# Optimization experiments

Measured on AMD Instinct MI355X. Metric: run time of the kernel, lower is better.

Reference implementation:

```python
import jax, jax.numpy as jnp
import numpy as np


def setup_inputs() -> dict:
    key = jax.random.key(0)
    ks = jax.random.split(key, 6)
    B, N, F, H, E = 2, 50000, 64, 32, 800000
    x = jax.random.normal(ks[0], (B, N, F), dtype=jnp.float32)
    edge_index = jax.random.randint(ks[1], (2, E), 0, N, dtype=jnp.int64)
    h_cur = jax.random.normal(ks[2], (B, N, H), dtype=jnp.float32)
    c_cur = jax.random.normal(ks[3], (B, N, H), dtype=jnp.float32)
    W = jax.random.normal(ks[4], (F + H, 4 * H), dtype=jnp.float32) * (1.0 / np.sqrt(F + H))
    b = jax.random.normal(ks[5], (4 * H,), dtype=jnp.float32) * 0.01
    return {"x": x, "edge_index": edge_index, "h_cur": h_cur, "c_cur": c_cur, "W": W, "b": b}


def reference(x, edge_index, h_cur, c_cur, W, b):
    B, N, _ = x.shape
    H = h_cur.shape[-1]

    # --- GCNConv on concatenated [x, h] ---
    combined = jnp.concatenate([x, h_cur], axis=-1)          # [B, N, F+H]
    xw = jnp.einsum('bnf,fg->bng', combined, W)              # [B, N, 4H]

    # add self-loops
    loop = jnp.arange(N, dtype=edge_index.dtype)
    src = jnp.concatenate([edge_index[0], loop])             # [E+N]
    dst = jnp.concatenate([edge_index[1], loop])             # [E+N]

    # symmetric degree normalization: deg over target index (PyG gcn_norm)
    deg = jnp.zeros((N,), dtype=xw.dtype).at[dst].add(1.0)
    dinv = jnp.where(deg > 0, jax.lax.rsqrt(deg), 0.0)
    norm = dinv[src] * dinv[dst]                             # [E+N]

    # gather-scale-scatter aggregation
    msgs = xw[:, src, :] * norm[None, :, None]               # [B, E+N, 4H]
    agg = jnp.zeros((B, N, 4 * H), dtype=xw.dtype).at[:, dst, :].add(msgs)
    conv = agg + b                                           # [B, N, 4H]

    # --- LSTM gating ---
    cc_i, cc_f, cc_o, cc_g = jnp.split(conv, 4, axis=-1)
    i = jax.nn.sigmoid(cc_i)
    f = jax.nn.sigmoid(cc_f)
    o = jax.nn.sigmoid(cc_o)
    g = jnp.tanh(cc_g)
    c_next = f * c_cur + i * g
    h_next = o * jnp.tanh(c_next)
    return h_next, c_next
```

## Files before the change

kernel.cpp:

```cpp
#include <hip/hip_runtime.h>
#include <hip/hip_bf16.h>

constexpr int G4H   = 128;
constexpr int H_DIM = 32;
constexpr int KPAD  = 104;
constexpr int CAP   = 64;

typedef __attribute__((ext_vector_type(8))) short bf16x8;
typedef __attribute__((ext_vector_type(4))) float f32x4;

static __device__ __forceinline__ unsigned short f2bf_bits(float v) {
    __hip_bfloat16 b = __float2bfloat16(v);
    return *reinterpret_cast<unsigned short*>(&b);
}
static __device__ __forceinline__ unsigned pack2(float a, float b) {
    return (unsigned)f2bf_bits(a) | ((unsigned)f2bf_bits(b) << 16);
}

static __device__ __forceinline__ void fma8(const uint4 u, float dsw, float* a)
{
    a[0] = fmaf(__uint_as_float(u.x << 16),         dsw, a[0]);
    a[1] = fmaf(__uint_as_float(u.x & 0xffff0000u), dsw, a[1]);
    a[2] = fmaf(__uint_as_float(u.y << 16),         dsw, a[2]);
    a[3] = fmaf(__uint_as_float(u.y & 0xffff0000u), dsw, a[3]);
    a[4] = fmaf(__uint_as_float(u.z << 16),         dsw, a[4]);
    a[5] = fmaf(__uint_as_float(u.z & 0xffff0000u), dsw, a[5]);
    a[6] = fmaf(__uint_as_float(u.w << 16),         dsw, a[6]);
    a[7] = fmaf(__uint_as_float(u.w & 0xffff0000u), dsw, a[7]);
}

__global__ __launch_bounds__(256)
void prep_kernel(const float* __restrict__ W,
                 unsigned short* __restrict__ Wt_g,
                 unsigned* __restrict__ cnt, int N)
{
    int gt = blockIdx.x * 256 + threadIdx.x;
    if (gt < N) cnt[gt] = 0u;
    if (gt < 96 * G4H) {
        int k = gt >> 7;
        int n = gt & 127;
        Wt_g[n * 96 + k] = f2bf_bits(W[gt]);
    }
}

__global__ __launch_bounds__(256)
void xw_fill_kernel(const float* __restrict__ x,
                    const float* __restrict__ h,
                    const unsigned short* __restrict__ Wt_g,
                    __hip_bfloat16* __restrict__ xw,
                    const int* __restrict__ ei,
                    unsigned* __restrict__ cnt,
                    unsigned short* __restrict__ bucket,
                    int BN, int E, int gemm_grid)
{
    const int bi = blockIdx.x;
    const int k3 = bi / 3;
    const int r3 = bi - 3 * k3;

    if (r3 != 0) {
        int f = 2 * k3 + r3 - 1;
        int e = f * 256 + threadIdx.x;
        if (e < E) {
            int dst = ei[E + e];
            unsigned pos = atomicAdd(&cnt[dst], 1u);
            if (pos < CAP) bucket[(long)dst * CAP + pos] = (unsigned short)ei[e];
        }
        return;
    }

    const int tile = k3;
    if (tile >= gemm_grid) return;

    __shared__ __align__(16) unsigned short smem[64 * 128];
    unsigned* smem_u = (unsigned*)smem;
    const int t = threadIdx.x;
    const long row0 = (long)tile * 64;

    #pragma unroll
    for (int j = 0; j < 4; ++j) {
        int i = t + 256 * j;
        int r = i >> 4, c4 = i & 15;
        long bn = row0 + r;
        float4 v = make_float4(0.f, 0.f, 0.f, 0.f);
        if (bn < BN) v = *reinterpret_cast<const float4*>(x + bn * 64 + 4 * c4);
        int base = r * KPAD + 4 * c4;
        smem_u[(base >> 1) + 0] = pack2(v.x, v.y);
        smem_u[(base >> 1) + 1] = pack2(v.z, v.w);
    }
    #pragma unroll
    for (int j = 0; j < 2; ++j) {
        int i = t + 256 * j;
        int r = i >> 3, c4 = i & 7;
        long bn = row0 + r;
        float4 v = make_float4(0.f, 0.f, 0.f, 0.f);
        if (bn < BN) v = *reinterpret_cast<const float4*>(h + bn * 32 + 4 * c4);
        int base = r * KPAD + 64 + 4 * c4;
        smem_u[(base >> 1) + 0] = pack2(v.x, v.y);
        smem_u[(base >> 1) + 1] = pack2(v.z, v.w);
    }
    __syncthreads();

    const int wv   = t >> 6;
    const int lane = t & 63;
    const int m    = lane & 15;
    const int q    = lane >> 4;

    f32x4 acc[8] = {};
    #pragma unroll
    for (int k0 = 0; k0 < 96; k0 += 32) {
        bf16x8 a = *reinterpret_cast<const bf16x8*>(&smem[(wv * 16 + m) * KPAD + k0 + q * 8]);
        #pragma unroll
        for (int nt = 0; nt < 8; ++nt) {
            bf16x8 b = *reinterpret_cast<const bf16x8*>(&Wt_g[(nt * 16 + m) * 96 + k0 + q * 8]);
            acc[nt] = __builtin_amdgcn_mfma_f32_16x16x32_bf16(a, b, acc[nt], 0, 0, 0);
        }
    }
    __syncthreads();

    #pragma unroll
    for (int nt = 0; nt < 8; ++nt) {
        #pragma unroll
        for (int r = 0; r < 4; ++r)
            smem[(wv * 16 + q * 4 + r) * 128 + nt * 16 + m] = f2bf_bits(acc[nt][r]);
    }
    __syncthreads();

    #pragma unroll
    for (int j = 0; j < 4; ++j) {
        int i = t + 256 * j;
        int r = i >> 4, c8 = i & 15;
        long bn = row0 + r;
        if (bn < BN) {
            uint4 v = *reinterpret_cast<const uint4*>(&smem[r * 128 + 8 * c8]);
            *reinterpret_cast<uint4*>(reinterpret_cast<unsigned short*>(xw) + bn * 128 + 8 * c8) = v;
        }
    }
}

__global__ __launch_bounds__(256)
void gather_gate_kernel(const unsigned* __restrict__ cnt,
                        const unsigned short* __restrict__ bucket,
                        const __hip_bfloat16* __restrict__ xw,
                        const float* __restrict__ bias,
                        const float* __restrict__ c_cur,
                        float* __restrict__ out,
                        int N)
{
    __shared__ float cc_lds[4][256];

    const int wid  = (int)(((long)blockIdx.x * 256 + threadIdx.x) >> 6);
    const int wv   = (threadIdx.x >> 6) & 3;
    const int lane = threadIdx.x & 63;
    const int g    = lane >> 4;
    const int w    = lane & 15;
    const bool live = (wid < N);
    const int n = live ? wid : 0;

    const int dn = live ? min((int)cnt[n], CAP) : 0;
    const unsigned short* __restrict__ brow = bucket + (long)n * CAP;

    float acc[16];
    #pragma unroll
    for (int j = 0; j < 16; ++j) acc[j] = 0.f;

    const __hip_bfloat16* __restrict__ xw0 = xw + (long)8 * w;
    const __hip_bfloat16* __restrict__ xw1 = xw + (long)N * G4H + 8 * w;

    for (int base = 0; base < dn; base += 64) {
        int cnt64 = min(64, dn - base);
        int   s_reg = 0;
        float d_reg = 0.f;
        if (lane < cnt64) {
            s_reg = (int)brow[base + lane];
            d_reg = rsqrtf((float)cnt[s_reg] + 1.f);
        }
        for (int i = 0; i < cnt64; i += 8) {
            int idx0 = i + g;
            int idx1 = i + 4 + g;
            int   src0 = __shfl(s_reg, idx0);
            float dsw0 = __shfl(d_reg, idx0);
            int   src1 = __shfl(s_reg, idx1);
            float dsw1 = __shfl(d_reg, idx1);
            if (idx0 >= cnt64) dsw0 = 0.f;
            if (idx1 >= cnt64) dsw1 = 0.f;
            uint4 a0 = *reinterpret_cast<const uint4*>(xw0 + (long)src0 * G4H);
            uint4 a1 = *reinterpret_cast<const uint4*>(xw1 + (long)src0 * G4H);
            uint4 b0 = *reinterpret_cast<const uint4*>(xw0 + (long)src1 * G4H);
            uint4 b1 = *reinterpret_cast<const uint4*>(xw1 + (long)src1 * G4H);
            fma8(a0, dsw0, acc);
            fma8(a1, dsw0, acc + 8);
            fma8(b0, dsw1, acc);
            fma8(b1, dsw1, acc + 8);
        }
    }

    #pragma unroll
    for (int j = 0; j < 16; ++j) {
        acc[j] += __shfl_xor(acc[j], 16);
        acc[j] += __shfl_xor(acc[j], 32);
    }

    float di = live ? rsqrtf((float)cnt[n] + 1.f) : 0.f;
    uint4 s0 = *reinterpret_cast<const uint4*>(xw0 + (long)n * G4H);
    uint4 s1 = *reinterpret_cast<const uint4*>(xw1 + (long)n * G4H);
    float sf[16];
    #pragma unroll
    for (int j = 0; j < 16; ++j) sf[j] = 0.f;
    fma8(s0, di, sf);
    fma8(s1, di, sf + 8);
    if (g == 0) {
        #pragma unroll
        for (int j = 0; j < 8; ++j) {
            float bj = bias[8 * w + j];
            cc_lds[wv][      8 * w + j] = di * (acc[j]     + sf[j])     + bj;
            cc_lds[wv][128 + 8 * w + j] = di * (acc[8 + j] + sf[8 + j]) + bj;
        }
    }
    __syncthreads();

    const int b = lane >> 5;
    const int l = lane & 31;
    float cc0 = cc_lds[wv][b * 128 + l];
    float cc1 = cc_lds[wv][b * 128 + l + 32];
    float cc2 = cc_lds[wv][b * 128 + l + 64];
    float cc3 = cc_lds[wv][b * 128 + l + 96];

    float ig = 1.f / (1.f + __expf(-cc0));
    float fg = 1.f / (1.f + __expf(-cc1));
    float og = 1.f / (1.f + __expf(-cc2));
    float gg = tanhf(cc3);

    if (live) {
        long t = ((long)b * N + n) * H_DIM + l;
        float c  = c_cur[t];
        float cn = fmaf(fg, c, ig * gg);
        float hn = og * tanhf(cn);
        out[t]                        = hn;
        out[(long)2 * N * H_DIM + t]  = cn;
    }
}

extern "C" void kernel_launch(void* const* d_in, const int* in_sizes, int n_in,
                              void* d_out, int out_size, void* d_ws, size_t ws_size,
                              hipStream_t stream)
{
    const float* x    = (const float*)d_in[0];
    const int*   ei   = (const int*)d_in[1];
    const float* h    = (const float*)d_in[2];
    const float* c    = (const float*)d_in[3];
    const float* W    = (const float*)d_in[4];
    const float* bias = (const float*)d_in[5];

    const int  E  = in_sizes[1] / 2;
    const long BN = (long)in_sizes[2] / H_DIM;
    const int  N  = (int)(BN / 2);

    char* ws = (char*)d_ws;
    __hip_bfloat16* xw = (__hip_bfloat16*)ws;
    size_t off = (size_t)BN * G4H * sizeof(__hip_bfloat16);
    unsigned* cnt = (unsigned*)(ws + off);   off += (size_t)N * sizeof(unsigned);
    unsigned short* bucket = (unsigned short*)(ws + off); off += (size_t)N * CAP * sizeof(unsigned short);
    unsigned short* Wt_g = (unsigned short*)(ws + off);   off += 96 * G4H * sizeof(unsigned short);

    int prep_grid = (max(N, 96 * G4H) + 255) / 256;
    prep_kernel<<<prep_grid, 256, 0, stream>>>(W, Wt_g, cnt, N);

    int gemm_grid = (int)((BN + 63) / 64);
    xw_fill_kernel<<<3 * gemm_grid, 256, 0, stream>>>(
        x, h, Wt_g, xw, ei, cnt, bucket, (int)BN, E, gemm_grid);

    int gg_grid = (N * 64 + 255) / 256;
    gather_gate_kernel<<<gg_grid, 256, 0, stream>>>(
        cnt, bucket, xw, bias, c, (float*)d_out, N);
}
```

Baseline: 207.0 us.

## Aggregate raw inputs before GEMM and fuse GEMM with LSTM gating

Uses linearity to reorder the work: the 96-wide bf16 input features (x and h, both batches interleaved) are gathered and normalized first, and the 128-wide projection through W is applied afterward. That projection is fused with the bias and LSTM gate math in one MFMA kernel. The gather now moves 96 packed bf16x2 words per source instead of two 128-wide rows, which cuts gather traffic, and the gate step no longer needs an LDS round trip. The cost is an extra kernel launch, an intermediate aggregated buffer, and some idle lanes (w>=24) in the gather.

```diff
diff --git a/kernel.cpp b/kernel.cpp
--- a/kernel.cpp
+++ b/kernel.cpp
@@ -1,7 +1,6 @@
 #include <hip/hip_runtime.h>
 #include <hip/hip_bf16.h>
 
-constexpr int G4H   = 128;
 constexpr int H_DIM = 32;
 constexpr int KPAD  = 104;
 constexpr int CAP   = 64;
@@ -16,50 +15,47 @@
 static __device__ __forceinline__ unsigned pack2(float a, float b) {
     return (unsigned)f2bf_bits(a) | ((unsigned)f2bf_bits(b) << 16);
 }
-
-static __device__ __forceinline__ void fma8(const uint4 u, float dsw, float* a)
-{
-    a[0] = fmaf(__uint_as_float(u.x << 16),         dsw, a[0]);
-    a[1] = fmaf(__uint_as_float(u.x & 0xffff0000u), dsw, a[1]);
-    a[2] = fmaf(__uint_as_float(u.y << 16),         dsw, a[2]);
-    a[3] = fmaf(__uint_as_float(u.y & 0xffff0000u), dsw, a[3]);
-    a[4] = fmaf(__uint_as_float(u.z << 16),         dsw, a[4]);
-    a[5] = fmaf(__uint_as_float(u.z & 0xffff0000u), dsw, a[5]);
-    a[6] = fmaf(__uint_as_float(u.w << 16),         dsw, a[6]);
-    a[7] = fmaf(__uint_as_float(u.w & 0xffff0000u), dsw, a[7]);
+static __device__ __forceinline__ float lo_f(unsigned u) { return __uint_as_float(u << 16); }
+static __device__ __forceinline__ float hi_f(unsigned u) { return __uint_as_float(u & 0xffff0000u); }
+
+static __device__ __forceinline__ void fma4p(const uint4 u, float d, float* a)
+{
+    a[0] = fmaf(lo_f(u.x), d, a[0]);
+    a[4] = fmaf(hi_f(u.x), d, a[4]);
+    a[1] = fmaf(lo_f(u.y), d, a[1]);
+    a[5] = fmaf(hi_f(u.y), d, a[5]);
+    a[2] = fmaf(lo_f(u.z), d, a[2]);
+    a[6] = fmaf(hi_f(u.z), d, a[6]);
+    a[3] = fmaf(lo_f(u.w), d, a[3]);
+    a[7] = fmaf(hi_f(u.w), d, a[7]);
 }
 
 __global__ __launch_bounds__(256)
 void prep_kernel(const float* __restrict__ W,
-                 unsigned short* __restrict__ Wt_g,
+                 unsigned short* __restrict__ Wt,
                  unsigned* __restrict__ cnt, int N)
 {
     int gt = blockIdx.x * 256 + threadIdx.x;
     if (gt < N) cnt[gt] = 0u;
-    if (gt < 96 * G4H) {
+    if (gt < 96 * 128) {
         int k = gt >> 7;
         int n = gt & 127;
-        Wt_g[n * 96 + k] = f2bf_bits(W[gt]);
-    }
-}
-
-__global__ __launch_bounds__(256)
-void xw_fill_kernel(const float* __restrict__ x,
-                    const float* __restrict__ h,
-                    const unsigned short* __restrict__ Wt_g,
-                    __hip_bfloat16* __restrict__ xw,
-                    const int* __restrict__ ei,
-                    unsigned* __restrict__ cnt,
-                    unsigned short* __restrict__ bucket,
-                    int BN, int E, int gemm_grid)
+        Wt[n * 96 + k] = f2bf_bits(W[gt]);
+    }
+}
+
+__global__ __launch_bounds__(256)
+void fill_convert_kernel(const float* __restrict__ x,
+                         const float* __restrict__ h,
+                         const int* __restrict__ ei,
+                         unsigned* __restrict__ cnt,
+                         unsigned short* __restrict__ bucket,
+                         unsigned* __restrict__ z,
+                         int N, int E, int fillGrid)
 {
     const int bi = blockIdx.x;
-    const int k3 = bi / 3;
-    const int r3 = bi - 3 * k3;
-
-    if (r3 != 0) {
-        int f = 2 * k3 + r3 - 1;
-        int e = f * 256 + threadIdx.x;
+    if (bi < fillGrid) {
+        int e = bi * 256 + threadIdx.x;
         if (e < E) {
             int dst = ei[E + e];
             unsigned pos = atomicAdd(&cnt[dst], 1u);
@@ -67,104 +63,47 @@
         }
         return;
     }
-
-    const int tile = k3;
-    if (tile >= gemm_grid) return;
-
-    __shared__ __align__(16) unsigned short smem[64 * 128];
-    unsigned* smem_u = (unsigned*)smem;
-    const int t = threadIdx.x;
-    const long row0 = (long)tile * 64;
-
-    #pragma unroll
-    for (int j = 0; j < 4; ++j) {
-        int i = t + 256 * j;
-        int r = i >> 4, c4 = i & 15;
-        long bn = row0 + r;
-        float4 v = make_float4(0.f, 0.f, 0.f, 0.f);
-        if (bn < BN) v = *reinterpret_cast<const float4*>(x + bn * 64 + 4 * c4);
-        int base = r * KPAD + 4 * c4;
-        smem_u[(base >> 1) + 0] = pack2(v.x, v.y);
-        smem_u[(base >> 1) + 1] = pack2(v.z, v.w);
-    }
-    #pragma unroll
-    for (int j = 0; j < 2; ++j) {
-        int i = t + 256 * j;
-        int r = i >> 3, c4 = i & 7;
-        long bn = row0 + r;
-        float4 v = make_float4(0.f, 0.f, 0.f, 0.f);
-        if (bn < BN) v = *reinterpret_cast<const float4*>(h + bn * 32 + 4 * c4);
-        int base = r * KPAD + 64 + 4 * c4;
-        smem_u[(base >> 1) + 0] = pack2(v.x, v.y);
-        smem_u[(base >> 1) + 1] = pack2(v.z, v.w);
-    }
-    __syncthreads();
-
-    const int wv   = t >> 6;
-    const int lane = t & 63;
-    const int m    = lane & 15;
-    const int q    = lane >> 4;
-
-    f32x4 acc[8] = {};
-    #pragma unroll
-    for (int k0 = 0; k0 < 96; k0 += 32) {
-        bf16x8 a = *reinterpret_cast<const bf16x8*>(&smem[(wv * 16 + m) * KPAD + k0 + q * 8]);
-        #pragma unroll
-        for (int nt = 0; nt < 8; ++nt) {
-            bf16x8 b = *reinterpret_cast<const bf16x8*>(&Wt_g[(nt * 16 + m) * 96 + k0 + q * 8]);
-            acc[nt] = __builtin_amdgcn_mfma_f32_16x16x32_bf16(a, b, acc[nt], 0, 0, 0);
-        }
-    }
-    __syncthreads();
-
-    #pragma unroll
-    for (int nt = 0; nt < 8; ++nt) {
-        #pragma unroll
-        for (int r = 0; r < 4; ++r)
-            smem[(wv * 16 + q * 4 + r) * 128 + nt * 16 + m] = f2bf_bits(acc[nt][r]);
-    }
-    __syncthreads();
-
-    #pragma unroll
-    for (int j = 0; j < 4; ++j) {
-        int i = t + 256 * j;
-        int r = i >> 4, c8 = i & 15;
-        long bn = row0 + r;
-        if (bn < BN) {
-            uint4 v = *reinterpret_cast<const uint4*>(&smem[r * 128 + 8 * c8]);
-            *reinterpret_cast<uint4*>(reinterpret_cast<unsigned short*>(xw) + bn * 128 + 8 * c8) = v;
-        }
-    }
-}
-
-__global__ __launch_bounds__(256)
-void gather_gate_kernel(const unsigned* __restrict__ cnt,
-                        const unsigned short* __restrict__ bucket,
-                        const __hip_bfloat16* __restrict__ xw,
-                        const float* __restrict__ bias,
-                        const float* __restrict__ c_cur,
-                        float* __restrict__ out,
-                        int N)
-{
-    __shared__ float cc_lds[4][256];
-
+    long idx = (long)(bi - fillGrid) * 256 + threadIdx.x;
+    if (idx >= (long)N * 24) return;
+    int n  = (int)(idx / 24);
+    int ku = (int)(idx - (long)n * 24);
+    int f0 = 4 * ku;
+    float4 a, b;
+    if (f0 < 64) {
+        a = *reinterpret_cast<const float4*>(x + (long)n * 64 + f0);
+        b = *reinterpret_cast<const float4*>(x + ((long)N + n) * 64 + f0);
+    } else {
+        a = *reinterpret_cast<const float4*>(h + (long)n * 32 + (f0 - 64));
+        b = *reinterpret_cast<const float4*>(h + ((long)N + n) * 32 + (f0 - 64));
+    }
+    uint4 o;
+    o.x = pack2(a.x, b.x);
+    o.y = pack2(a.y, b.y);
+    o.z = pack2(a.z, b.z);
+    o.w = pack2(a.w, b.w);
+    *reinterpret_cast<uint4*>(z + idx * 4) = o;
+}
+
+__global__ __launch_bounds__(256)
+void gather_kernel(const unsigned* __restrict__ cnt,
+                   const unsigned short* __restrict__ bucket,
+                   const unsigned* __restrict__ z,
+                   unsigned* __restrict__ aggz, int N)
+{
     const int wid  = (int)(((long)blockIdx.x * 256 + threadIdx.x) >> 6);
-    const int wv   = (threadIdx.x >> 6) & 3;
     const int lane = threadIdx.x & 63;
-    const int g    = lane >> 4;
-    const int w    = lane & 15;
+    const int g    = lane >> 5;
+    const int w    = lane & 31;
     const bool live = (wid < N);
     const int n = live ? wid : 0;
 
     const int dn = live ? min((int)cnt[n], CAP) : 0;
     const unsigned short* __restrict__ brow = bucket + (long)n * CAP;
-
-    float acc[16];
-    #pragma unroll
-    for (int j = 0; j < 16; ++j) acc[j] = 0.f;
-
-    const __hip_bfloat16* __restrict__ xw0 = xw + (long)8 * w;
-    const __hip_bfloat16* __restrict__ xw1 = xw + (long)N * G4H + 8 * w;
+    const unsigned* __restrict__ zw = z + 4 * w;
+
+    float acc[8];
+    #pragma unroll
+    for (int j = 0; j < 8; ++j) acc[j] = 0.f;
 
     for (int base = 0; base < dn; base += 64) {
         int cnt64 = min(64, dn - base);
@@ -175,68 +114,122 @@
             d_reg = rsqrtf((float)cnt[s_reg] + 1.f);
         }
         for (int i = 0; i < cnt64; i += 8) {
-            int idx0 = i + g;
-            int idx1 = i + 4 + g;
-            int   src0 = __shfl(s_reg, idx0);
-            float dsw0 = __shfl(d_reg, idx0);
-            int   src1 = __shfl(s_reg, idx1);
-            float dsw1 = __shfl(d_reg, idx1);
-            if (idx0 >= cnt64) dsw0 = 0.f;
-            if (idx1 >= cnt64) dsw1 = 0.f;
-            uint4 a0 = *reinterpret_cast<const uint4*>(xw0 + (long)src0 * G4H);
-            uint4 a1 = *reinterpret_cast<const uint4*>(xw1 + (long)src0 * G4H);
-            uint4 b0 = *reinterpret_cast<const uint4*>(xw0 + (long)src1 * G4H);
-            uint4 b1 = *reinterpret_cast<const uint4*>(xw1 + (long)src1 * G4H);
-            fma8(a0, dsw0, acc);
-            fma8(a1, dsw0, acc + 8);
-            fma8(b0, dsw1, acc);
-            fma8(b1, dsw1, acc + 8);
-        }
-    }
-
-    #pragma unroll
-    for (int j = 0; j < 16; ++j) {
-        acc[j] += __shfl_xor(acc[j], 16);
-        acc[j] += __shfl_xor(acc[j], 32);
-    }
-
-    float di = live ? rsqrtf((float)cnt[n] + 1.f) : 0.f;
-    uint4 s0 = *reinterpret_cast<const uint4*>(xw0 + (long)n * G4H);
-    uint4 s1 = *reinterpret_cast<const uint4*>(xw1 + (long)n * G4H);
-    float sf[16];
-    #pragma unroll
-    for (int j = 0; j < 16; ++j) sf[j] = 0.f;
-    fma8(s0, di, sf);
-    fma8(s1, di, sf + 8);
-    if (g == 0) {
+            int i0 = i + g, i1 = i + 2 + g, i2 = i + 4 + g, i3 = i + 6 + g;
+            int   s0 = __shfl(s_reg, i0);  float d0 = __shfl(d_reg, i0);
+            int   s1 = __shfl(s_reg, i1);  float d1 = __shfl(d_reg, i1);
+            int   s2 = __shfl(s_reg, i2);  float d2 = __shfl(d_reg, i2);
+            int   s3 = __shfl(s_reg, i3);  float d3 = __shfl(d_reg, i3);
+            if (i0 >= cnt64) d0 = 0.f;
+            if (i1 >= cnt64) d1 = 0.f;
+            if (i2 >= cnt64) d2 = 0.f;
+            if (i3 >= cnt64) d3 = 0.f;
+            uint4 u0 = make_uint4(0,0,0,0), u1 = u0, u2 = u0, u3 = u0;
+            if (w < 24) {
+                u0 = *reinterpret_cast<const uint4*>(zw + (long)s0 * 96);
+                u1 = *reinterpret_cast<const uint4*>(zw + (long)s1 * 96);
+                u2 = *reinterpret_cast<const uint4*>(zw + (long)s2 * 96);
+                u3 = *reinterpret_cast<const uint4*>(zw + (long)s3 * 96);
+            }
+            fma4p(u0, d0, acc);
+            fma4p(u1, d1, acc);
+            fma4p(u2, d2, acc);
+            fma4p(u3, d3, acc);
+        }
+    }
+
+    #pragma unroll
+    for (int j = 0; j < 8; ++j) acc[j] += __shfl_xor(acc[j], 32);
+
+    if (live && g == 0 && w < 24) {
+        float di  = rsqrtf((float)cnt[n] + 1.f);
+        float di2 = di * di;
+        uint4 us = *reinterpret_cast<const uint4*>(zw + (long)n * 96);
+        uint4 o;
+        o.x = pack2(fmaf(di, acc[0], di2 * lo_f(us.x)), fmaf(di, acc[4], di2 * hi_f(us.x)));
+        o.y = pack2(fmaf(di, acc[1], di2 * lo_f(us.y)), fmaf(di, acc[5], di2 * hi_f(us.y)));
+        o.z = pack2(fmaf(di, acc[2], di2 * lo_f(us.z)), fmaf(di, acc[6], di2 * hi_f(us.z)));
+        o.w = pack2(fmaf(di, acc[3], di2 * lo_f(us.w)), fmaf(di, acc[7], di2 * hi_f(us.w)));
+        *reinterpret_cast<uint4*>(aggz + (long)n * 96 + 4 * w) = o;
+    }
+}
+
+__global__ __launch_bounds__(256)
+void gemm_gates_kernel(const unsigned* __restrict__ aggz,
+                       const unsigned short* __restrict__ Wt,
+                       const float* __restrict__ bias,
+                       const float* __restrict__ c_cur,
+                       float* __restrict__ out,
+                       int N)
+{
+    __shared__ __align__(16) unsigned short As[64 * KPAD];
+    const int t  = threadIdx.x;
+    const int n0 = blockIdx.x * 32;
+
+    #pragma unroll
+    for (int j = 0; j < 3; ++j) {
+        int idx = t + 256 * j;
+        int i   = idx / 24;
+        int ku  = idx - 24 * i;
+        int n   = n0 + i;
+        uint4 u = make_uint4(0,0,0,0);
+        if (n < N) u = *reinterpret_cast<const uint4*>(aggz + (long)n * 96 + 4 * ku);
+        ushort4 lo, hi;
+        lo.x = (unsigned short)u.x;  hi.x = (unsigned short)(u.x >> 16);
+        lo.y = (unsigned short)u.y;  hi.y = (unsigned short)(u.y >> 16);
+        lo.z = (unsigned short)u.z;  hi.z = (unsigned short)(u.z >> 16);
+        lo.w = (unsigned short)u.w;  hi.w = (unsigned short)(u.w >> 16);
+        *reinterpret_cast<ushort4*>(&As[i * KPAD + 4 * ku])        = lo;
+        *reinterpret_cast<ushort4*>(&As[(32 + i) * KPAD + 4 * ku]) = hi;
+    }
+    __syncthreads();
+
+    const int wv   = t >> 6;
+    const int lane = t & 63;
+    const int m    = lane & 15;
+    const int q    = lane >> 4;
+
+    f32x4 acc[8] = {};
+    #pragma unroll
+    for (int k0 = 0; k0 < 96; k0 += 32) {
+        bf16x8 a = *reinterpret_cast<const bf16x8*>(&As[(wv * 16 + m) * KPAD + k0 + q * 8]);
         #pragma unroll
-        for (int j = 0; j < 8; ++j) {
-            float bj = bias[8 * w + j];
-            cc_lds[wv][      8 * w + j] = di * (acc[j]     + sf[j])     + bj;
-            cc_lds[wv][128 + 8 * w + j] = di * (acc[8 + j] + sf[8 + j]) + bj;
-        }
-    }
-    __syncthreads();
-
-    const int b = lane >> 5;
-    const int l = lane & 31;
-    float cc0 = cc_lds[wv][b * 128 + l];
-    float cc1 = cc_lds[wv][b * 128 + l + 32];
-    float cc2 = cc_lds[wv][b * 128 + l + 64];
-    float cc3 = cc_lds[wv][b * 128 + l + 96];
-
-    float ig = 1.f / (1.f + __expf(-cc0));
-    float fg = 1.f / (1.f + __expf(-cc1));
-    float og = 1.f / (1.f + __expf(-cc2));
-    float gg = tanhf(cc3);
-
-    if (live) {
-        long t = ((long)b * N + n) * H_DIM + l;
-        float c  = c_cur[t];
-        float cn = fmaf(fg, c, ig * gg);
-        float hn = og * tanhf(cn);
-        out[t]                        = hn;
-        out[(long)2 * N * H_DIM + t]  = cn;
+        for (int nt = 0; nt < 8; ++nt) {
+            bf16x8 b = *reinterpret_cast<const bf16x8*>(&Wt[(nt * 16 + m) * 96 + k0 + q * 8]);
+            acc[nt] = __builtin_amdgcn_mfma_f32_16x16x32_bf16(a, b, acc[nt], 0, 0, 0);
+        }
+    }
+
+    const float bi0 = bias[m],       bi1 = bias[16 + m];
+    const float bf0 = bias[32 + m],  bf1 = bias[48 + m];
+    const float bo0 = bias[64 + m],  bo1 = bias[80 + m];
+    const float bg0 = bias[96 + m],  bg1 = bias[112 + m];
+    const long  co  = (long)2 * N * H_DIM;
+
+    #pragma unroll
+    for (int r = 0; r < 4; ++r) {
+        int rr = wv * 16 + q * 4 + r;
+        int b  = rr >> 5;
+        int i  = rr & 31;
+        int n  = n0 + i;
+        if (n < N) {
+            long base = ((long)b * N + n) * H_DIM;
+            float c0 = c_cur[base + m];
+            float c1 = c_cur[base + 16 + m];
+            float ig0 = 1.f / (1.f + __expf(-(acc[0][r] + bi0)));
+            float ig1 = 1.f / (1.f + __expf(-(acc[1][r] + bi1)));
+            float fg0 = 1.f / (1.f + __expf(-(acc[2][r] + bf0)));
+            float fg1 = 1.f / (1.f + __expf(-(acc[3][r] + bf1)));
+            float og0 = 1.f / (1.f + __expf(-(acc[4][r] + bo0)));
+            float og1 = 1.f / (1.f + __expf(-(acc[5][r] + bo1)));
+            float gg0 = tanhf(acc[6][r] + bg0);
+            float gg1 = tanhf(acc[7][r] + bg1);
+            float cn0 = fmaf(fg0, c0, ig0 * gg0);
+            float cn1 = fmaf(fg1, c1, ig1 * gg1);
+            out[base + m]           = og0 * tanhf(cn0);
+            out[base + 16 + m]      = og1 * tanhf(cn1);
+            out[co + base + m]      = cn0;
+            out[co + base + 16 + m] = cn1;
+        }
     }
 }
 
@@ -256,20 +249,24 @@
     const int  N  = (int)(BN / 2);
 
     char* ws = (char*)d_ws;
-    __hip_bfloat16* xw = (__hip_bfloat16*)ws;
-    size_t off = (size_t)BN * G4H * sizeof(__hip_bfloat16);
-    unsigned* cnt = (unsigned*)(ws + off);   off += (size_t)N * sizeof(unsigned);
+    unsigned* z = (unsigned*)ws;
+    size_t off = (size_t)N * 96 * sizeof(unsigned);
+    unsigned* aggz = (unsigned*)(ws + off);  off += (size_t)N * 96 * sizeof(unsigned);
+    unsigned* cnt  = (unsigned*)(ws + off);  off += (size_t)N * sizeof(unsigned);
     unsigned short* bucket = (unsigned short*)(ws + off); off += (size_t)N * CAP * sizeof(unsigned short);
-    unsigned short* Wt_g = (unsigned short*)(ws + off);   off += 96 * G4H * sizeof(unsigned short);
-
-    int prep_grid = (max(N, 96 * G4H) + 255) / 256;
-    prep_kernel<<<prep_grid, 256, 0, stream>>>(W, Wt_g, cnt, N);
-
-    int gemm_grid = (int)((BN + 63) / 64);
-    xw_fill_kernel<<<3 * gemm_grid, 256, 0, stream>>>(
-        x, h, Wt_g, xw, ei, cnt, bucket, (int)BN, E, gemm_grid);
-
-    int gg_grid = (N * 64 + 255) / 256;
-    gather_gate_kernel<<<gg_grid, 256, 0, stream>>>(
-        cnt, bucket, xw, bias, c, (float*)d_out, N);
-}
+    unsigned short* Wt = (unsigned short*)(ws + off);     off += 96 * 128 * sizeof(unsigned short);
+
+    int prep_grid = (max(N, 96 * 128) + 255) / 256;
+    prep_kernel<<<prep_grid, 256, 0, stream>>>(W, Wt, cnt, N);
+
+    int fillGrid = (E + 255) / 256;
+    int convGrid = (int)(((long)N * 24 + 255) / 256);
+    fill_convert_kernel<<<fillGrid + convGrid, 256, 0, stream>>>(
+        x, h, ei, cnt, bucket, z, N, E, fillGrid);
+
+    int gGrid = (int)(((long)N * 64 + 255) / 256);
+    gather_kernel<<<gGrid, 256, 0, stream>>>(cnt, bucket, z, aggz, N);
+
+    int mGrid = (N + 31) / 32;
+    gemm_gates_kernel<<<mGrid, 256, 0, stream>>>(aggz, Wt, bias, c, (float*)d_out, N);
+}
```

After: 209.1 us. No clear change (+1.0%).
